# Optimization experiments

Hardware: AMD Instinct MI355X
Metric: run time of the kernel (lower is better)

## Reference

```python
import jax, jax.numpy as jnp
import numpy as np

H = 1024
NH = 16
HD = H // NH
TEMP = 0.5
LN_EPS = 1e-5


def setup_inputs() -> dict:
    key = jax.random.key(0)
    ks = jax.random.split(key, 11)
    s = 1.0 / np.sqrt(H)
    return {
        "feat": jax.random.normal(ks[0], (4, 2048, H), dtype=jnp.float32),
        "qw": jax.random.uniform(ks[1], (H, H), jnp.float32, -s, s),
        "qb": jax.random.uniform(ks[2], (H,), jnp.float32, -s, s),
        "kw": jax.random.uniform(ks[3], (H, H), jnp.float32, -s, s),
        "kb": jax.random.uniform(ks[4], (H,), jnp.float32, -s, s),
        "vw": jax.random.uniform(ks[5], (H, H), jnp.float32, -s, s),
        "vb": jax.random.uniform(ks[6], (H,), jnp.float32, -s, s),
        "ow": jax.random.uniform(ks[7], (H, H), jnp.float32, -s, s),
        "ob": jax.random.uniform(ks[8], (H,), jnp.float32, -s, s),
        "ln_g": jnp.ones((H,), jnp.float32),
        "ln_b": jnp.zeros((H,), jnp.float32),
    }


def reference(feat, qw, qb, kw, kb, vw, vb, ow, ob, ln_g, ln_b):
    B, S, _ = feat.shape
    # torch Linear: y = x @ W.T + b
    def split_heads(x):  # [B,S,H] -> [B,NH,S,HD]
        return x.reshape(B, S, NH, HD).transpose(0, 2, 1, 3)

    Q = split_heads(feat @ qw.T + qb)
    K = split_heads(feat @ kw.T + kb)
    V = split_heads(feat @ vw.T + vb)

    # temperature-scaled attention (note: divide by 0.5, NOT 1/sqrt(d))
    scores = jnp.einsum("bhqd,bhkd->bhqk", Q, K) / TEMP
    w = jax.nn.softmax(scores, axis=-1)
    attn = jnp.einsum("bhqk,bhkd->bhqd", w, V)  # [B,NH,S,HD]
    attn = attn.transpose(0, 2, 1, 3).reshape(B, S, H)

    out = attn @ ow.T + ob
    out = jax.nn.relu(out)  # dropout is identity in eval mode
    mu = jnp.mean(out, axis=-1, keepdims=True)
    var = jnp.mean(jnp.square(out - mu), axis=-1, keepdims=True)
    out = (out - mu) * jax.lax.rsqrt(var + LN_EPS) * ln_g + ln_b
    return out
```

## Files before the change

kernel.cpp:

```cpp
#include <hip/hip_runtime.h>
#include <math.h>

#define HDIM 1024
#define NHEAD 16
#define HEADD 64
#define SEQLEN 2048
#define BATCH 4
#define MROWS (BATCH * SEQLEN)
#define LN_EPS 1e-5f

typedef float f32x4 __attribute__((ext_vector_type(4)));
typedef short s16x8 __attribute__((ext_vector_type(8)));
typedef short s16x4 __attribute__((ext_vector_type(4)));
typedef __bf16 bf16x4 __attribute__((ext_vector_type(4)));

#define MFMA16(a, b, c) __builtin_amdgcn_mfma_f32_16x16x32_bf16((a), (b), (c), 0, 0, 0)

__device__ __forceinline__ void load_lds16(const __bf16* g, __bf16* l) {
  __builtin_amdgcn_global_load_lds((const __attribute__((address_space(1))) void*)g,
                                   (__attribute__((address_space(3))) void*)l, 16, 0, 0);
}

__global__ __launch_bounds__(256) void split_k(const float* __restrict__ src,
                                               __bf16* __restrict__ h,
                                               __bf16* __restrict__ l, int n4) {
  int i = blockIdx.x * blockDim.x + threadIdx.x;
  if (i >= n4) return;
  float4 v = reinterpret_cast<const float4*>(src)[i];
  bf16x4 hv, lv;
  hv[0] = (__bf16)v.x; hv[1] = (__bf16)v.y; hv[2] = (__bf16)v.z; hv[3] = (__bf16)v.w;
  lv[0] = (__bf16)(v.x - (float)hv[0]);
  lv[1] = (__bf16)(v.y - (float)hv[1]);
  lv[2] = (__bf16)(v.z - (float)hv[2]);
  lv[3] = (__bf16)(v.w - (float)hv[3]);
  reinterpret_cast<bf16x4*>(h)[i] = hv;
  reinterpret_cast<bf16x4*>(l)[i] = lv;
}

template <int EPI, int PASSES>
__global__ __launch_bounds__(256, 2) void gemm3p_k(
    const __bf16* __restrict__ AH, const __bf16* __restrict__ AL,
    const __bf16* __restrict__ BH, const __bf16* __restrict__ BL,
    const float* __restrict__ bias, __bf16* __restrict__ CH,
    __bf16* __restrict__ CL, float* __restrict__ CF) {
  __shared__ __bf16 smem[32768];

  const int tid = threadIdx.x;
  const int lane = tid & 63;
  const int w = tid >> 6;
  const int fr = lane & 15;
  const int g = lane >> 4;
  const int wm = w >> 1, wn = w & 1;
  const int m0 = blockIdx.x << 7;
  const int n0 = blockIdx.y << 7;

#define GSTAGE(buf, kt)                                                       \
  do {                                                                        \
    const int ke_ = (kt) * 32 + (lane & 3) * 8;                               \
    _Pragma("unroll") for (int c_ = 0; c_ < 2; ++c_) {                        \
      const int rr_ = 32 * w + 16 * c_ + (lane >> 2);                         \
      const int lo_ = (32 * w + 16 * c_) * 32;                                \
      load_lds16(AH + (size_t)(m0 + rr_) * HDIM + ke_, &smem[(buf)*4096 + lo_]); \
      load_lds16(AL + (size_t)(m0 + rr_) * HDIM + ke_, &smem[8192 + (buf)*4096 + lo_]); \
      load_lds16(BH + (size_t)(n0 + rr_) * HDIM + ke_, &smem[16384 + (buf)*4096 + lo_]); \
      if (PASSES == 3)                                                        \
        load_lds16(BL + (size_t)(n0 + rr_) * HDIM + ke_, &smem[24576 + (buf)*4096 + lo_]); \
    }                                                                         \
  } while (0)

  f32x4 acc[4][4] = {};

  GSTAGE(0, 0);
  __syncthreads();

  for (int kt = 0; kt < HDIM / 32; ++kt) {
    const int buf = kt & 1;
    if (kt + 1 < HDIM / 32) GSTAGE(buf ^ 1, kt + 1);

    s16x8 aH[4], aL[4], bH[4], bL[4];
#pragma unroll
    for (int mi = 0; mi < 4; ++mi) {
      const int off = (wm * 64 + mi * 16 + fr) * 32 + g * 8;
      aH[mi] = *reinterpret_cast<const s16x8*>(&smem[buf * 4096 + off]);
      aL[mi] = *reinterpret_cast<const s16x8*>(&smem[8192 + buf * 4096 + off]);
    }
#pragma unroll
    for (int ni = 0; ni < 4; ++ni) {
      const int off = (wn * 64 + ni * 16 + fr) * 32 + g * 8;
      bH[ni] = *reinterpret_cast<const s16x8*>(&smem[16384 + buf * 4096 + off]);
      if (PASSES == 3)
        bL[ni] = *reinterpret_cast<const s16x8*>(&smem[24576 + buf * 4096 + off]);
    }
#pragma unroll
    for (int mi = 0; mi < 4; ++mi)
#pragma unroll
      for (int ni = 0; ni < 4; ++ni) {
        acc[mi][ni] = MFMA16(aH[mi], bH[ni], acc[mi][ni]);
        if (PASSES == 3) acc[mi][ni] = MFMA16(aH[mi], bL[ni], acc[mi][ni]);
        acc[mi][ni] = MFMA16(aL[mi], bH[ni], acc[mi][ni]);
      }
    __syncthreads();
  }

  float bv[4];
#pragma unroll
  for (int ni = 0; ni < 4; ++ni) bv[ni] = bias[n0 + wn * 64 + ni * 16 + fr];

  if (EPI == 0) {
#pragma unroll
    for (int mi = 0; mi < 4; ++mi)
#pragma unroll
      for (int ni = 0; ni < 4; ++ni)
#pragma unroll
        for (int r = 0; r < 4; ++r) {
          const float v = acc[mi][ni][r] + bv[ni];
          const int m = m0 + wm * 64 + mi * 16 + 4 * g + r;
          const int n = n0 + wn * 64 + ni * 16 + fr;
          const int b = m >> 11, s = m & 2047, h = n >> 6, d = n & 63;
          const size_t o = ((size_t)(b * NHEAD + h) * SEQLEN + s) * HEADD + d;
          const __bf16 hb = (__bf16)v;
          CH[o] = hb;
          CL[o] = (__bf16)(v - (float)hb);
        }
  } else if (EPI == 2) {
#pragma unroll
    for (int mi = 0; mi < 4; ++mi)
#pragma unroll
      for (int ni = 0; ni < 4; ++ni)
#pragma unroll
        for (int r = 0; r < 4; ++r) {
          const int m = m0 + wm * 64 + mi * 16 + 4 * g + r;
          const int n = n0 + wn * 64 + ni * 16 + fr;
          CF[(size_t)m * HDIM + n] = acc[mi][ni][r] + bv[ni];
        }
  } else {
    __syncthreads();
#pragma unroll
    for (int mi = 0; mi < 4; ++mi)
#pragma unroll
      for (int ni = 0; ni < 4; ++ni)
#pragma unroll
        for (int r = 0; r < 4; ++r) {
          const float v = acc[mi][ni][r] + bv[ni];
          const int nl = wn * 64 + ni * 16 + fr;
          const int ml = wm * 64 + mi * 16 + 4 * g + r;
          smem[nl * 128 + (((ml >> 3) ^ (nl & 7)) << 3) + (ml & 7)] = (__bf16)v;
        }
    __syncthreads();
    const int nl = tid >> 1, mh = tid & 1;
    const int b = m0 >> 11, s0 = m0 & 2047;
    const int gn = n0 + nl, h = gn >> 6, d = gn & 63;
#pragma unroll
    for (int j = 0; j < 8; ++j) {
      const int cm = mh * 8 + j;
      s16x8 vv = *reinterpret_cast<const s16x8*>(&smem[nl * 128 + ((cm ^ (nl & 7)) << 3)]);
      const size_t o = ((size_t)((b * NHEAD + h) * HEADD + d)) * SEQLEN + s0 + cm * 8;
      *reinterpret_cast<s16x8*>(&CH[o]) = vv;
    }
  }
#undef GSTAGE
}

__global__ __launch_bounds__(256, 2) void attn5_k(
    const __bf16* __restrict__ QH, const __bf16* __restrict__ QL,
    const __bf16* __restrict__ KH, const __bf16* __restrict__ KL,
    const __bf16* __restrict__ VT, __bf16* __restrict__ OH,
    __bf16* __restrict__ OL) {
  __shared__ __bf16 smem[32768];

  const int tid = threadIdx.x;
  const int lane = tid & 63;
  const int w = tid >> 6;
  const int fr = lane & 15;
  const int g = lane >> 4;
  const int f7 = fr & 7;

  const int blk = blockIdx.x;
  const int xcd = blk & 7, idx = blk >> 3;
  const int bh = xcd * 8 + (idx >> 4);
  const int qt = idx & 15;
  const int q0 = qt << 7;
  const size_t bhO = (size_t)bh * SEQLEN * HEADD;

  s16x8 qHf[2][2], qLf[2][2];
#pragma unroll
  for (int qb = 0; qb < 2; ++qb) {
    const size_t qoff = bhO + (size_t)(q0 + w * 32 + qb * 16 + fr) * HEADD;
#pragma unroll
    for (int ks = 0; ks < 2; ++ks) {
      qHf[qb][ks] = *reinterpret_cast<const s16x8*>(&QH[qoff + ks * 32 + g * 8]);
      qLf[qb][ks] = *reinterpret_cast<const s16x8*>(&QL[qoff + ks * 32 + g * 8]);
    }
  }

#define ASTAGE(buf, kt)                                                        \
  do {                                                                         \
    const int kv0_ = (kt) * 64;                                                \
    const int rsub_ = lane >> 3;                                               \
    const int ch_ = (lane & 7) ^ rsub_;                                        \
    _Pragma("unroll") for (int i_ = 0; i_ < 6; ++i_) {                         \
      const int L_ = w * 6 + i_;                                               \
      const int t_ = L_ >> 3, sub_ = L_ & 7;                                   \
      __bf16* lp_ = &smem[t_ * 8192 + (buf)*4096 + sub_ * 512];                \
      if (t_ < 2) {                                                            \
        const __bf16* base_ = (t_ == 0) ? KH : KL;                             \
        load_lds16(base_ + bhO + (size_t)(kv0_ + sub_ * 8 + rsub_) * HEADD + ch_ * 8, lp_); \
      } else {                                                                 \
        load_lds16(VT + ((size_t)bh * HEADD + sub_ * 8 + rsub_) * SEQLEN + kv0_ + ch_ * 8, lp_); \
      }                                                                        \
    }                                                                          \
  } while (0)

  f32x4 oacc[2][4] = {};
  float m_run[2] = {-1e30f, -1e30f};
  float l_run[2] = {0.f, 0.f};

  ASTAGE(0, 0);
  __syncthreads();

  for (int kt = 0; kt < SEQLEN / 64; ++kt) {
    const int buf = kt & 1;
    if (kt + 1 < SEQLEN / 64) ASTAGE(buf ^ 1, kt + 1);

    f32x4 sf[2][4] = {};
    __builtin_amdgcn_s_setprio(1);
#pragma unroll
    for (int kb = 0; kb < 4; ++kb) {
      s16x8 kh[2], kl[2];
#pragma unroll
      for (int ks = 0; ks < 2; ++ks) {
        const int off = (kb * 16 + fr) * 64 + (((ks * 4 + g) ^ f7) << 3);
        kh[ks] = *reinterpret_cast<const s16x8*>(&smem[buf * 4096 + off]);
        kl[ks] = *reinterpret_cast<const s16x8*>(&smem[8192 + buf * 4096 + off]);
      }
#pragma unroll
      for (int qb = 0; qb < 2; ++qb)
#pragma unroll
        for (int ks = 0; ks < 2; ++ks) {
          sf[qb][kb] = MFMA16(kh[ks], qHf[qb][ks], sf[qb][kb]);
          sf[qb][kb] = MFMA16(kl[ks], qHf[qb][ks], sf[qb][kb]);
          sf[qb][kb] = MFMA16(kh[ks], qLf[qb][ks], sf[qb][kb]);
        }
    }
    __builtin_amdgcn_s_setprio(0);

    float mxa[2];
#pragma unroll
    for (int qb = 0; qb < 2; ++qb) {
      float mx = -1e30f;
#pragma unroll
      for (int kb = 0; kb < 4; ++kb) {
        sf[qb][kb] *= 2.0f;
#pragma unroll
        for (int r = 0; r < 4; ++r) mx = fmaxf(mx, sf[qb][kb][r]);
      }
      mx = fmaxf(mx, __shfl_xor(mx, 16));
      mx = fmaxf(mx, __shfl_xor(mx, 32));
      mxa[qb] = mx;
    }
    const bool ok = (mxa[0] <= m_run[0] + 8.f) && (mxa[1] <= m_run[1] + 8.f);
    if (!__all(ok)) {
#pragma unroll
      for (int qb = 0; qb < 2; ++qb) {
        const float mn = fmaxf(m_run[qb], mxa[qb]);
        const float corr = __expf(m_run[qb] - mn);
        m_run[qb] = mn;
        l_run[qb] *= corr;
        float cr[4];
#pragma unroll
        for (int r = 0; r < 4; ++r) cr[r] = __shfl(corr, 4 * g + r);
#pragma unroll
        for (int di = 0; di < 4; ++di)
#pragma unroll
          for (int r = 0; r < 4; ++r) oacc[qb][di][r] *= cr[r];
      }
    }
#pragma unroll
    for (int qb = 0; qb < 2; ++qb) {
      float ps = 0.f;
#pragma unroll
      for (int kb = 0; kb < 4; ++kb)
#pragma unroll
        for (int r = 0; r < 4; ++r) {
          const float p = __expf(sf[qb][kb][r] - m_run[qb]);
          sf[qb][kb][r] = p;
          ps += p;
        }
      ps += __shfl_xor(ps, 16);
      ps += __shfl_xor(ps, 32);
      l_run[qb] += ps;
    }

#pragma unroll
    for (int qb = 0; qb < 2; ++qb) {
      const int q = w * 32 + qb * 16 + fr;
#pragma unroll
      for (int kb = 0; kb < 4; ++kb) {
        s16x4 hh;
#pragma unroll
        for (int r = 0; r < 4; ++r)
          hh[r] = __builtin_bit_cast(short, (__bf16)sf[qb][kb][r]);
        const int cd = 2 * kb + (g >> 1);
        const int off = q * 64 + ((cd ^ f7) << 3) + (g & 1) * 4;
        *reinterpret_cast<s16x4*>(&smem[24576 + off]) = hh;
      }
    }

    __builtin_amdgcn_s_setprio(1);
#pragma unroll
    for (int ks = 0; ks < 2; ++ks) {
      s16x8 pH[2];
#pragma unroll
      for (int qb = 0; qb < 2; ++qb) {
        const int q = w * 32 + qb * 16 + fr;
        const int off = q * 64 + (((ks * 4 + g) ^ f7) << 3);
        pH[qb] = *reinterpret_cast<const s16x8*>(&smem[24576 + off]);
      }
#pragma unroll
      for (int di = 0; di < 4; ++di) {
        const int d = di * 16 + fr;
        const int voff = d * 64 + (((ks * 4 + g) ^ f7) << 3);
        s16x8 vf = *reinterpret_cast<const s16x8*>(&smem[16384 + buf * 4096 + voff]);
#pragma unroll
        for (int qb = 0; qb < 2; ++qb)
          oacc[qb][di] = MFMA16(pH[qb], vf, oacc[qb][di]);
      }
    }
    __builtin_amdgcn_s_setprio(0);
    __syncthreads();
  }

  const int b = bh >> 4, h = bh & 15;
#pragma unroll
  for (int qb = 0; qb < 2; ++qb) {
    const float inv = 1.0f / l_run[qb];
    float iv[4];
#pragma unroll
    for (int r = 0; r < 4; ++r) iv[r] = __shfl(inv, 4 * g + r);
#pragma unroll
    for (int di = 0; di < 4; ++di)
#pragma unroll
      for (int r = 0; r < 4; ++r) {
        const float v = oacc[qb][di][r] * iv[r];
        const int srow = q0 + w * 32 + qb * 16 + 4 * g + r;
        const size_t o = ((size_t)b * SEQLEN + srow) * HDIM + h * 64 + di * 16 + fr;
        const __bf16 hb = (__bf16)v;
        OH[o] = hb;
        OL[o] = (__bf16)(v - (float)hb);
      }
  }
#undef ASTAGE
}

__global__ __launch_bounds__(256) void relu_ln_k(const float* __restrict__ X,
                                                 const float* __restrict__ gam,
                                                 const float* __restrict__ bta,
                                                 float* __restrict__ out) {
  __shared__ float red[8];
  const int row = blockIdx.x;
  const int tid = threadIdx.x;
  const int c = tid << 2;

  const float4 v = *reinterpret_cast<const float4*>(&X[(size_t)row * HDIM + c]);
  float x[4] = {fmaxf(v.x, 0.f), fmaxf(v.y, 0.f), fmaxf(v.z, 0.f), fmaxf(v.w, 0.f)};
  float sum = x[0] + x[1] + x[2] + x[3];
  float ss = x[0] * x[0] + x[1] * x[1] + x[2] * x[2] + x[3] * x[3];
#pragma unroll
  for (int off = 1; off < 64; off <<= 1) {
    sum += __shfl_xor(sum, off);
    ss += __shfl_xor(ss, off);
  }
  const int wid = tid >> 6;
  if ((tid & 63) == 0) {
    red[wid] = sum;
    red[4 + wid] = ss;
  }
  __syncthreads();
  sum = red[0] + red[1] + red[2] + red[3];
  ss = red[4] + red[5] + red[6] + red[7];
  const float mean = sum * (1.0f / HDIM);
  const float var = ss * (1.0f / HDIM) - mean * mean;
  const float rstd = rsqrtf(var + LN_EPS);

  const float4 gv = *reinterpret_cast<const float4*>(&gam[c]);
  const float4 bv = *reinterpret_cast<const float4*>(&bta[c]);
  float4 o;
  o.x = (x[0] - mean) * rstd * gv.x + bv.x;
  o.y = (x[1] - mean) * rstd * gv.y + bv.y;
  o.z = (x[2] - mean) * rstd * gv.z + bv.z;
  o.w = (x[3] - mean) * rstd * gv.w + bv.w;
  *reinterpret_cast<float4*>(&out[(size_t)row * HDIM + c]) = o;
}

extern "C" void kernel_launch(void* const* d_in, const int* in_sizes, int n_in,
                              void* d_out, int out_size, void* d_ws, size_t ws_size,
                              hipStream_t stream) {
  const float* feat = (const float*)d_in[0];
  const float* qw = (const float*)d_in[1];
  const float* qb = (const float*)d_in[2];
  const float* kw = (const float*)d_in[3];
  const float* kb = (const float*)d_in[4];
  const float* vw = (const float*)d_in[5];
  const float* vb = (const float*)d_in[6];
  const float* ow = (const float*)d_in[7];
  const float* ob = (const float*)d_in[8];
  const float* ln_g = (const float*)d_in[9];
  const float* ln_b = (const float*)d_in[10];

  char* ws = (char*)d_ws;
  const size_t MB = 1u << 20;
  __bf16* qwH = (__bf16*)(ws + 0 * MB);
  __bf16* kwH = (__bf16*)(ws + 2 * MB);
  __bf16* vwH = (__bf16*)(ws + 4 * MB);
  __bf16* owH = (__bf16*)(ws + 6 * MB);
  __bf16* qwL = (__bf16*)(ws + 8 * MB);
  __bf16* kwL = (__bf16*)(ws + 10 * MB);
  __bf16* vwL = (__bf16*)(ws + 12 * MB);
  __bf16* owL = (__bf16*)(ws + 14 * MB);
  __bf16* QHp = (__bf16*)(ws + 16 * MB);
  __bf16* QLp = (__bf16*)(ws + 32 * MB);
  __bf16* KHp = (__bf16*)(ws + 48 * MB);
  __bf16* KLp = (__bf16*)(ws + 64 * MB);
  __bf16* VTp = (__bf16*)(ws + 80 * MB);
  __bf16* ftH = (__bf16*)(ws + 96 * MB);
  __bf16* ftL = (__bf16*)(ws + 112 * MB);
  __bf16* atH = ftH;
  __bf16* atL = ftL;
  float* proj = (float*)(ws + 16 * MB);

  split_k<<<(MROWS * HDIM / 4 + 255) / 256, 256, 0, stream>>>(feat, ftH, ftL, MROWS * HDIM / 4);
  split_k<<<(HDIM * HDIM / 4 + 255) / 256, 256, 0, stream>>>(qw, qwH, qwL, HDIM * HDIM / 4);
  split_k<<<(HDIM * HDIM / 4 + 255) / 256, 256, 0, stream>>>(kw, kwH, kwL, HDIM * HDIM / 4);
  split_k<<<(HDIM * HDIM / 4 + 255) / 256, 256, 0, stream>>>(vw, vwH, vwL, HDIM * HDIM / 4);
  split_k<<<(HDIM * HDIM / 4 + 255) / 256, 256, 0, stream>>>(ow, owH, owL, HDIM * HDIM / 4);

  const dim3 gg(MROWS / 128, HDIM / 128);
  gemm3p_k<0, 3><<<gg, 256, 0, stream>>>(ftH, ftL, qwH, qwL, qb, QHp, QLp, nullptr);
  gemm3p_k<0, 3><<<gg, 256, 0, stream>>>(ftH, ftL, kwH, kwL, kb, KHp, KLp, nullptr);
  gemm3p_k<1, 2><<<gg, 256, 0, stream>>>(ftH, ftL, vwH, vwL, vb, VTp, nullptr, nullptr);

  attn5_k<<<BATCH * NHEAD * (SEQLEN / 128), 256, 0, stream>>>(QHp, QLp, KHp, KLp, VTp, atH, atL);

  gemm3p_k<2, 2><<<gg, 256, 0, stream>>>(atH, atL, owH, owL, ob, nullptr, nullptr, proj);

  relu_ln_k<<<MROWS, 256, 0, stream>>>(proj, ln_g, ln_b, (float*)d_out);
}
```

Baseline: 457.2 us.

## Fold softmax scale into Q, use exp2, restructure attention loop, merge weight splits

Q is pre-scaled by 2*log2(e) in the projection epilogue so the attention kernel can use native exp2 with no per-score multiply, and the lazy-rescale threshold is adjusted to match. The attention kernel now uses precomputed per-thread global/LDS addresses with pointer increments, a two-step unrolled double-buffer loop, and a per-wave P buffer layout. The four weight-split launches become one 2D launch, and the 2-pass GEMM uses smaller LDS and requests 3 blocks per CU. Each piece targets instruction count or launch overhead, at the risk of register pressure and changed rounding from scaling Q before the bf16 split.

```diff
diff --git a/kernel.cpp b/kernel.cpp
--- a/kernel.cpp
+++ b/kernel.cpp
@@ -8,6 +8,7 @@
 #define BATCH 4
 #define MROWS (BATCH * SEQLEN)
 #define LN_EPS 1e-5f
+#define QSCALE 2.8853900817779268f
 
 typedef float f32x4 __attribute__((ext_vector_type(4)));
 typedef short s16x8 __attribute__((ext_vector_type(8)));
@@ -15,6 +16,12 @@
 typedef __bf16 bf16x4 __attribute__((ext_vector_type(4)));
 
 #define MFMA16(a, b, c) __builtin_amdgcn_mfma_f32_16x16x32_bf16((a), (b), (c), 0, 0, 0)
+
+#if __has_builtin(__builtin_amdgcn_exp2f)
+#define EXP2(x) __builtin_amdgcn_exp2f(x)
+#else
+#define EXP2(x) exp2f(x)
+#endif
 
 __device__ __forceinline__ void load_lds16(const __bf16* g, __bf16* l) {
   __builtin_amdgcn_global_load_lds((const __attribute__((address_space(1))) void*)g,
@@ -37,13 +44,35 @@
   reinterpret_cast<bf16x4*>(l)[i] = lv;
 }
 
+__global__ __launch_bounds__(256) void wsplit_k(
+    const float* __restrict__ w0, const float* __restrict__ w1,
+    const float* __restrict__ w2, const float* __restrict__ w3,
+    __bf16* __restrict__ h0, __bf16* __restrict__ l0, __bf16* __restrict__ h1,
+    __bf16* __restrict__ l1, __bf16* __restrict__ h2, __bf16* __restrict__ l2,
+    __bf16* __restrict__ h3, __bf16* __restrict__ l3) {
+  const int which = blockIdx.y;
+  const float* src = which == 0 ? w0 : which == 1 ? w1 : which == 2 ? w2 : w3;
+  __bf16* h = which == 0 ? h0 : which == 1 ? h1 : which == 2 ? h2 : h3;
+  __bf16* l = which == 0 ? l0 : which == 1 ? l1 : which == 2 ? l2 : l3;
+  const int i = blockIdx.x * blockDim.x + threadIdx.x;
+  float4 v = reinterpret_cast<const float4*>(src)[i];
+  bf16x4 hv, lv;
+  hv[0] = (__bf16)v.x; hv[1] = (__bf16)v.y; hv[2] = (__bf16)v.z; hv[3] = (__bf16)v.w;
+  lv[0] = (__bf16)(v.x - (float)hv[0]);
+  lv[1] = (__bf16)(v.y - (float)hv[1]);
+  lv[2] = (__bf16)(v.z - (float)hv[2]);
+  lv[3] = (__bf16)(v.w - (float)hv[3]);
+  reinterpret_cast<bf16x4*>(h)[i] = hv;
+  reinterpret_cast<bf16x4*>(l)[i] = lv;
+}
+
 template <int EPI, int PASSES>
-__global__ __launch_bounds__(256, 2) void gemm3p_k(
+__global__ __launch_bounds__(256, PASSES == 2 ? 3 : 2) void gemm3p_k(
     const __bf16* __restrict__ AH, const __bf16* __restrict__ AL,
     const __bf16* __restrict__ BH, const __bf16* __restrict__ BL,
-    const float* __restrict__ bias, __bf16* __restrict__ CH,
+    const float* __restrict__ bias, const float scale, __bf16* __restrict__ CH,
     __bf16* __restrict__ CL, float* __restrict__ CF) {
-  __shared__ __bf16 smem[32768];
+  __shared__ __bf16 smem[(PASSES == 3) ? 32768 : 24576];
 
   const int tid = threadIdx.x;
   const int lane = tid & 63;
@@ -113,7 +142,7 @@
       for (int ni = 0; ni < 4; ++ni)
 #pragma unroll
         for (int r = 0; r < 4; ++r) {
-          const float v = acc[mi][ni][r] + bv[ni];
+          const float v = (acc[mi][ni][r] + bv[ni]) * scale;
           const int m = m0 + wm * 64 + mi * 16 + 4 * g + r;
           const int n = n0 + wn * 64 + ni * 16 + fr;
           const int b = m >> 11, s = m & 2047, h = n >> 6, d = n & 63;
@@ -161,7 +190,7 @@
 #undef GSTAGE
 }
 
-__global__ __launch_bounds__(256, 2) void attn5_k(
+__global__ __launch_bounds__(256, 2) void attn6_k(
     const __bf16* __restrict__ QH, const __bf16* __restrict__ QL,
     const __bf16* __restrict__ KH, const __bf16* __restrict__ KL,
     const __bf16* __restrict__ VT, __bf16* __restrict__ OH,
@@ -193,162 +222,189 @@
     }
   }
 
-#define ASTAGE(buf, kt)                                                        \
-  do {                                                                         \
-    const int kv0_ = (kt) * 64;                                                \
-    const int rsub_ = lane >> 3;                                               \
-    const int ch_ = (lane & 7) ^ rsub_;                                        \
-    _Pragma("unroll") for (int i_ = 0; i_ < 6; ++i_) {                         \
-      const int L_ = w * 6 + i_;                                               \
-      const int t_ = L_ >> 3, sub_ = L_ & 7;                                   \
-      __bf16* lp_ = &smem[t_ * 8192 + (buf)*4096 + sub_ * 512];                \
-      if (t_ < 2) {                                                            \
-        const __bf16* base_ = (t_ == 0) ? KH : KL;                             \
-        load_lds16(base_ + bhO + (size_t)(kv0_ + sub_ * 8 + rsub_) * HEADD + ch_ * 8, lp_); \
-      } else {                                                                 \
-        load_lds16(VT + ((size_t)bh * HEADD + sub_ * 8 + rsub_) * SEQLEN + kv0_ + ch_ * 8, lp_); \
-      }                                                                        \
-    }                                                                          \
+  const __bf16* gsrc[6];
+  int gstep[6], ldoff[6];
+  {
+    const int rsub = lane >> 3;
+    const int ch = (lane & 7) ^ rsub;
+#pragma unroll
+    for (int i_ = 0; i_ < 6; ++i_) {
+      const int L_ = w * 6 + i_;
+      const int t_ = L_ >> 3, sub_ = L_ & 7;
+      ldoff[i_] = t_ * 8192 + sub_ * 512;
+      if (t_ < 2) {
+        const __bf16* base_ = (t_ == 0) ? KH : KL;
+        gsrc[i_] = base_ + bhO + (size_t)(sub_ * 8 + rsub) * HEADD + ch * 8;
+        gstep[i_] = 64 * HEADD;
+      } else {
+        gsrc[i_] = VT + ((size_t)bh * HEADD + sub_ * 8 + rsub) * SEQLEN + ch * 8;
+        gstep[i_] = 64;
+      }
+    }
+  }
+
+#define ASTAGE(bufl)                                              \
+  do {                                                            \
+    _Pragma("unroll") for (int i_ = 0; i_ < 6; ++i_) {            \
+      load_lds16(gsrc[i_], &smem[ldoff[i_] + (bufl)*4096]);       \
+      gsrc[i_] += gstep[i_];                                      \
+    }                                                             \
   } while (0)
 
-  f32x4 oacc[2][4] = {};
-  float m_run[2] = {-1e30f, -1e30f};
-  float l_run[2] = {0.f, 0.f};
-
-  ASTAGE(0, 0);
+  const int rb0 = fr * 64 + ((g ^ f7) << 3);
+  const int rb1 = fr * 64 + (((4 + g) ^ f7) << 3);
+  const int prbase = 24576 + w * 2048;
+  const int pwbase = 24576 + w * 2048 + fr * 64 + (g & 1) * 4;
+  int pco[4];
+#pragma unroll
+  for (int kb = 0; kb < 4; ++kb) pco[kb] = ((2 * kb + (g >> 1)) ^ f7) << 3;
+
+  f32x4 oacc0[4] = {}, oacc1[4] = {};
+  float m0r = -1e30f, m1r = -1e30f, l0r = 0.f, l1r = 0.f;
+
+  auto process = [&](const int B) {
+    f32x4 sf0[4] = {}, sf1[4] = {};
+    __builtin_amdgcn_s_setprio(1);
+#pragma unroll
+    for (int kb = 0; kb < 4; ++kb) {
+      const s16x8 kh0 = *reinterpret_cast<const s16x8*>(&smem[B * 4096 + kb * 1024 + rb0]);
+      const s16x8 kl0 = *reinterpret_cast<const s16x8*>(&smem[8192 + B * 4096 + kb * 1024 + rb0]);
+      const s16x8 kh1 = *reinterpret_cast<const s16x8*>(&smem[B * 4096 + kb * 1024 + rb1]);
+      const s16x8 kl1 = *reinterpret_cast<const s16x8*>(&smem[8192 + B * 4096 + kb * 1024 + rb1]);
+      sf0[kb] = MFMA16(kh0, qHf[0][0], sf0[kb]);
+      sf0[kb] = MFMA16(kl0, qHf[0][0], sf0[kb]);
+      sf0[kb] = MFMA16(kh0, qLf[0][0], sf0[kb]);
+      sf0[kb] = MFMA16(kh1, qHf[0][1], sf0[kb]);
+      sf0[kb] = MFMA16(kl1, qHf[0][1], sf0[kb]);
+      sf0[kb] = MFMA16(kh1, qLf[0][1], sf0[kb]);
+      sf1[kb] = MFMA16(kh0, qHf[1][0], sf1[kb]);
+      sf1[kb] = MFMA16(kl0, qHf[1][0], sf1[kb]);
+      sf1[kb] = MFMA16(kh0, qLf[1][0], sf1[kb]);
+      sf1[kb] = MFMA16(kh1, qHf[1][1], sf1[kb]);
+      sf1[kb] = MFMA16(kl1, qHf[1][1], sf1[kb]);
+      sf1[kb] = MFMA16(kh1, qLf[1][1], sf1[kb]);
+    }
+    __builtin_amdgcn_s_setprio(0);
+
+    float mx0 = sf0[0][0], mx1 = sf1[0][0];
+#pragma unroll
+    for (int kb = 0; kb < 4; ++kb)
+#pragma unroll
+      for (int r = 0; r < 4; ++r) {
+        mx0 = fmaxf(mx0, sf0[kb][r]);
+        mx1 = fmaxf(mx1, sf1[kb][r]);
+      }
+    mx0 = fmaxf(mx0, __shfl_xor(mx0, 16));
+    mx0 = fmaxf(mx0, __shfl_xor(mx0, 32));
+    mx1 = fmaxf(mx1, __shfl_xor(mx1, 16));
+    mx1 = fmaxf(mx1, __shfl_xor(mx1, 32));
+    const bool ok = (mx0 <= m0r + 11.5f) && (mx1 <= m1r + 11.5f);
+    if (!__all(ok)) {
+      const float mn0 = fmaxf(m0r, mx0), mn1 = fmaxf(m1r, mx1);
+      const float c0 = EXP2(m0r - mn0), c1 = EXP2(m1r - mn1);
+      m0r = mn0; m1r = mn1;
+      l0r *= c0; l1r *= c1;
+      float cr0[4], cr1[4];
+#pragma unroll
+      for (int r = 0; r < 4; ++r) {
+        cr0[r] = __shfl(c0, 4 * g + r);
+        cr1[r] = __shfl(c1, 4 * g + r);
+      }
+#pragma unroll
+      for (int di = 0; di < 4; ++di)
+#pragma unroll
+        for (int r = 0; r < 4; ++r) {
+          oacc0[di][r] *= cr0[r];
+          oacc1[di][r] *= cr1[r];
+        }
+    }
+    float ps0 = 0.f, ps1 = 0.f;
+#pragma unroll
+    for (int kb = 0; kb < 4; ++kb)
+#pragma unroll
+      for (int r = 0; r < 4; ++r) {
+        const float p0 = EXP2(sf0[kb][r] - m0r);
+        const float p1 = EXP2(sf1[kb][r] - m1r);
+        sf0[kb][r] = p0;
+        sf1[kb][r] = p1;
+        ps0 += p0;
+        ps1 += p1;
+      }
+    ps0 += __shfl_xor(ps0, 16);
+    ps0 += __shfl_xor(ps0, 32);
+    ps1 += __shfl_xor(ps1, 16);
+    ps1 += __shfl_xor(ps1, 32);
+    l0r += ps0;
+    l1r += ps1;
+
+#pragma unroll
+    for (int kb = 0; kb < 4; ++kb) {
+      s16x4 h0, h1;
+#pragma unroll
+      for (int r = 0; r < 4; ++r) {
+        h0[r] = __builtin_bit_cast(short, (__bf16)sf0[kb][r]);
+        h1[r] = __builtin_bit_cast(short, (__bf16)sf1[kb][r]);
+      }
+      *reinterpret_cast<s16x4*>(&smem[pwbase + pco[kb]]) = h0;
+      *reinterpret_cast<s16x4*>(&smem[pwbase + 1024 + pco[kb]]) = h1;
+    }
+
+    __builtin_amdgcn_s_setprio(1);
+#pragma unroll
+    for (int ks = 0; ks < 2; ++ks) {
+      const int rbv = ks ? rb1 : rb0;
+      const s16x8 p0 = *reinterpret_cast<const s16x8*>(&smem[prbase + rbv]);
+      const s16x8 p1 = *reinterpret_cast<const s16x8*>(&smem[prbase + 1024 + rbv]);
+#pragma unroll
+      for (int di = 0; di < 4; ++di) {
+        const s16x8 vf = *reinterpret_cast<const s16x8*>(
+            &smem[16384 + B * 4096 + di * 1024 + rbv]);
+        oacc0[di] = MFMA16(p0, vf, oacc0[di]);
+        oacc1[di] = MFMA16(p1, vf, oacc1[di]);
+      }
+    }
+    __builtin_amdgcn_s_setprio(0);
+  };
+
+  ASTAGE(0);
   __syncthreads();
-
-  for (int kt = 0; kt < SEQLEN / 64; ++kt) {
-    const int buf = kt & 1;
-    if (kt + 1 < SEQLEN / 64) ASTAGE(buf ^ 1, kt + 1);
-
-    f32x4 sf[2][4] = {};
-    __builtin_amdgcn_s_setprio(1);
-#pragma unroll
-    for (int kb = 0; kb < 4; ++kb) {
-      s16x8 kh[2], kl[2];
-#pragma unroll
-      for (int ks = 0; ks < 2; ++ks) {
-        const int off = (kb * 16 + fr) * 64 + (((ks * 4 + g) ^ f7) << 3);
-        kh[ks] = *reinterpret_cast<const s16x8*>(&smem[buf * 4096 + off]);
-        kl[ks] = *reinterpret_cast<const s16x8*>(&smem[8192 + buf * 4096 + off]);
-      }
-#pragma unroll
-      for (int qb = 0; qb < 2; ++qb)
-#pragma unroll
-        for (int ks = 0; ks < 2; ++ks) {
-          sf[qb][kb] = MFMA16(kh[ks], qHf[qb][ks], sf[qb][kb]);
-          sf[qb][kb] = MFMA16(kl[ks], qHf[qb][ks], sf[qb][kb]);
-          sf[qb][kb] = MFMA16(kh[ks], qLf[qb][ks], sf[qb][kb]);
-        }
-    }
-    __builtin_amdgcn_s_setprio(0);
-
-    float mxa[2];
-#pragma unroll
-    for (int qb = 0; qb < 2; ++qb) {
-      float mx = -1e30f;
-#pragma unroll
-      for (int kb = 0; kb < 4; ++kb) {
-        sf[qb][kb] *= 2.0f;
-#pragma unroll
-        for (int r = 0; r < 4; ++r) mx = fmaxf(mx, sf[qb][kb][r]);
-      }
-      mx = fmaxf(mx, __shfl_xor(mx, 16));
-      mx = fmaxf(mx, __shfl_xor(mx, 32));
-      mxa[qb] = mx;
-    }
-    const bool ok = (mxa[0] <= m_run[0] + 8.f) && (mxa[1] <= m_run[1] + 8.f);
-    if (!__all(ok)) {
-#pragma unroll
-      for (int qb = 0; qb < 2; ++qb) {
-        const float mn = fmaxf(m_run[qb], mxa[qb]);
-        const float corr = __expf(m_run[qb] - mn);
-        m_run[qb] = mn;
-        l_run[qb] *= corr;
-        float cr[4];
-#pragma unroll
-        for (int r = 0; r < 4; ++r) cr[r] = __shfl(corr, 4 * g + r);
-#pragma unroll
-        for (int di = 0; di < 4; ++di)
-#pragma unroll
-          for (int r = 0; r < 4; ++r) oacc[qb][di][r] *= cr[r];
-      }
-    }
-#pragma unroll
-    for (int qb = 0; qb < 2; ++qb) {
-      float ps = 0.f;
-#pragma unroll
-      for (int kb = 0; kb < 4; ++kb)
-#pragma unroll
-        for (int r = 0; r < 4; ++r) {
-          const float p = __expf(sf[qb][kb][r] - m_run[qb]);
-          sf[qb][kb][r] = p;
-          ps += p;
-        }
-      ps += __shfl_xor(ps, 16);
-      ps += __shfl_xor(ps, 32);
-      l_run[qb] += ps;
-    }
-
-#pragma unroll
-    for (int qb = 0; qb < 2; ++qb) {
-      const int q = w * 32 + qb * 16 + fr;
-#pragma unroll
-      for (int kb = 0; kb < 4; ++kb) {
-        s16x4 hh;
-#pragma unroll
-        for (int r = 0; r < 4; ++r)
-          hh[r] = __builtin_bit_cast(short, (__bf16)sf[qb][kb][r]);
-        const int cd = 2 * kb + (g >> 1);
-        const int off = q * 64 + ((cd ^ f7) << 3) + (g & 1) * 4;
-        *reinterpret_cast<s16x4*>(&smem[24576 + off]) = hh;
-      }
-    }
-
-    __builtin_amdgcn_s_setprio(1);
-#pragma unroll
-    for (int ks = 0; ks < 2; ++ks) {
-      s16x8 pH[2];
-#pragma unroll
-      for (int qb = 0; qb < 2; ++qb) {
-        const int q = w * 32 + qb * 16 + fr;
-        const int off = q * 64 + (((ks * 4 + g) ^ f7) << 3);
-        pH[qb] = *reinterpret_cast<const s16x8*>(&smem[24576 + off]);
-      }
-#pragma unroll
-      for (int di = 0; di < 4; ++di) {
-        const int d = di * 16 + fr;
-        const int voff = d * 64 + (((ks * 4 + g) ^ f7) << 3);
-        s16x8 vf = *reinterpret_cast<const s16x8*>(&smem[16384 + buf * 4096 + voff]);
-#pragma unroll
-        for (int qb = 0; qb < 2; ++qb)
-          oacc[qb][di] = MFMA16(pH[qb], vf, oacc[qb][di]);
-      }
-    }
-    __builtin_amdgcn_s_setprio(0);
+  for (int kt = 0; kt < SEQLEN / 64 - 2; kt += 2) {
+    ASTAGE(1);
+    process(0);
     __syncthreads();
-  }
+    ASTAGE(0);
+    process(1);
+    __syncthreads();
+  }
+  ASTAGE(1);
+  process(0);
+  __syncthreads();
+  process(1);
 
   const int b = bh >> 4, h = bh & 15;
-#pragma unroll
-  for (int qb = 0; qb < 2; ++qb) {
-    const float inv = 1.0f / l_run[qb];
-    float iv[4];
-#pragma unroll
-    for (int r = 0; r < 4; ++r) iv[r] = __shfl(inv, 4 * g + r);
-#pragma unroll
-    for (int di = 0; di < 4; ++di)
-#pragma unroll
-      for (int r = 0; r < 4; ++r) {
-        const float v = oacc[qb][di][r] * iv[r];
-        const int srow = q0 + w * 32 + qb * 16 + 4 * g + r;
-        const size_t o = ((size_t)b * SEQLEN + srow) * HDIM + h * 64 + di * 16 + fr;
-        const __bf16 hb = (__bf16)v;
-        OH[o] = hb;
-        OL[o] = (__bf16)(v - (float)hb);
-      }
-  }
+  const float inv0 = 1.0f / l0r, inv1 = 1.0f / l1r;
+  float iv0[4], iv1[4];
+#pragma unroll
+  for (int r = 0; r < 4; ++r) {
+    iv0[r] = __shfl(inv0, 4 * g + r);
+    iv1[r] = __shfl(inv1, 4 * g + r);
+  }
+#pragma unroll
+  for (int di = 0; di < 4; ++di)
+#pragma unroll
+    for (int r = 0; r < 4; ++r) {
+      const int srow = q0 + w * 32 + 4 * g + r;
+      const size_t o0 = ((size_t)b * SEQLEN + srow) * HDIM + h * 64 + di * 16 + fr;
+      const size_t o1 = o0 + 16 * HDIM;
+      const float v0 = oacc0[di][r] * iv0[r];
+      const float v1 = oacc1[di][r] * iv1[r];
+      const __bf16 hb0 = (__bf16)v0;
+      const __bf16 hb1 = (__bf16)v1;
+      OH[o0] = hb0;
+      OL[o0] = (__bf16)(v0 - (float)hb0);
+      OH[o1] = hb1;
+      OL[o1] = (__bf16)(v1 - (float)hb1);
+    }
 #undef ASTAGE
 }
 
@@ -428,20 +484,21 @@
   __bf16* atL = ftL;
   float* proj = (float*)(ws + 16 * MB);
 
-  split_k<<<(MROWS * HDIM / 4 + 255) / 256, 256, 0, stream>>>(feat, ftH, ftL, MROWS * HDIM / 4);
-  split_k<<<(HDIM * HDIM / 4 + 255) / 256, 256, 0, stream>>>(qw, qwH, qwL, HDIM * HDIM / 4);
-  split_k<<<(HDIM * HDIM / 4 + 255) / 256, 256, 0, stream>>>(kw, kwH, kwL, HDIM * HDIM / 4);
-  split_k<<<(HDIM * HDIM / 4 + 255) / 256, 256, 0, stream>>>(vw, vwH, vwL, HDIM * HDIM / 4);
-  split_k<<<(HDIM * HDIM / 4 + 255) / 256, 256, 0, stream>>>(ow, owH, owL, HDIM * HDIM / 4);
+  split_k<<<(MROWS * HDIM / 4 + 255) / 256, 256, 0, stream>>>(feat, ftH, ftL,
+                                                              MROWS * HDIM / 4);
+  wsplit_k<<<dim3(HDIM * HDIM / 4 / 256, 4), 256, 0, stream>>>(
+      qw, kw, vw, ow, qwH, qwL, kwH, kwL, vwH, vwL, owH, owL);
 
   const dim3 gg(MROWS / 128, HDIM / 128);
-  gemm3p_k<0, 3><<<gg, 256, 0, stream>>>(ftH, ftL, qwH, qwL, qb, QHp, QLp, nullptr);
-  gemm3p_k<0, 3><<<gg, 256, 0, stream>>>(ftH, ftL, kwH, kwL, kb, KHp, KLp, nullptr);
-  gemm3p_k<1, 2><<<gg, 256, 0, stream>>>(ftH, ftL, vwH, vwL, vb, VTp, nullptr, nullptr);
-
-  attn5_k<<<BATCH * NHEAD * (SEQLEN / 128), 256, 0, stream>>>(QHp, QLp, KHp, KLp, VTp, atH, atL);
-
-  gemm3p_k<2, 2><<<gg, 256, 0, stream>>>(atH, atL, owH, owL, ob, nullptr, nullptr, proj);
+  gemm3p_k<0, 3><<<gg, 256, 0, stream>>>(ftH, ftL, qwH, qwL, qb, QSCALE, QHp, QLp, nullptr);
+  gemm3p_k<0, 3><<<gg, 256, 0, stream>>>(ftH, ftL, kwH, kwL, kb, 1.0f, KHp, KLp, nullptr);
+  gemm3p_k<1, 2><<<gg, 256, 0, stream>>>(ftH, ftL, vwH, vwL, vb, 1.0f, VTp, nullptr, nullptr);
+
+  attn6_k<<<BATCH * NHEAD * (SEQLEN / 128), 256, 0, stream>>>(QHp, QLp, KHp, KLp,
+                                                              VTp, atH, atL);
+
+  gemm3p_k<2, 2><<<gg, 256, 0, stream>>>(atH, atL, owH, owL, ob, 1.0f, nullptr,
+                                         nullptr, proj);
 
   relu_ln_k<<<MROWS, 256, 0, stream>>>(proj, ln_g, ln_b, (float*)d_out);
 }
```

Result: no change. 451.5 us (-1.2%).
